# Kernel tuning notes

Measured on AMD Instinct MI355X. Metric: run time of the kernel, lower is better.

## Reference

```python
import jax, jax.numpy as jnp
import numpy as np

NUM_ENT = 40000
NUM_REL = 100
EMBED_DIM = 256
FEAT_DIM = 768
BATCH = 32
SEQ_LEN = 3
MASK_POS = 2
EPS = 1e-12


def setup_inputs() -> dict:
    key = jax.random.key(0)
    k1, k2, k3, k4 = jax.random.split(key, 4)
    ent_pkl = jax.random.normal(k1, (NUM_ENT, FEAT_DIM), dtype=jnp.float32)
    other_emb = jax.random.normal(k2, (NUM_ENT + NUM_REL + 3 - NUM_ENT, EMBED_DIM), dtype=jnp.float32)
    proj_W = jax.random.normal(k3, (EMBED_DIM, FEAT_DIM), dtype=jnp.float32) * (1.0 / np.sqrt(FEAT_DIM))
    batch_input_ids = jax.random.randint(k4, (BATCH, SEQ_LEN), 0, NUM_ENT + NUM_REL + 3, dtype=jnp.int64)
    return {
        "ent_pkl": ent_pkl,
        "other_emb": other_emb,
        "proj_W": proj_W,
        "batch_input_ids": batch_input_ids,
        "batch_mask_position": MASK_POS,
    }


def reference(ent_pkl, other_emb, proj_W, batch_input_ids, batch_mask_position):
    # unity embeddings: [other[0], proj(ent_pkl), other[1:]] -> [num_ent+num_rel+3, d]
    ent_proj = ent_pkl @ proj_W.T  # Linear(feat_dim, embed_dim, bias=False)
    unity = jnp.concatenate([other_emb[:1], ent_proj, other_emb[1:]], axis=0)

    mp = int(batch_mask_position)
    # drop the masked slot, keep up to 3 tokens total -> [B, 2]
    query_input = jnp.concatenate(
        [batch_input_ids[:, :mp], batch_input_ids[:, mp + 1:3]], axis=1)
    query_emb = unity[query_input]  # [B, 2, d]
    # F.normalize(dim=-1): x / max(||x||_2, eps)
    norm = jnp.sqrt(jnp.sum(query_emb * query_emb, axis=-1, keepdims=True))
    query_emb = query_emb / jnp.maximum(norm, EPS)
    query_sum = jnp.sum(query_emb, axis=1)  # [B, d]

    E_embed = unity[:NUM_ENT + 1]  # [num_ent+1, d]
    # broadcast L1 distance: [B, num_ent+1]
    score = -jnp.sum(jnp.abs(query_sum[:, None, :] - E_embed[None, :, :]), axis=-1)
    return score
```

## Files before the change

### kernel.cpp

```cpp
#include <hip/hip_runtime.h>
#include <hip/hip_bf16.h>
#include <stdint.h>

#define NE 40000
#define FD 768
#define ED 256
#define NB 32
#define OUTC (NE + 1)

typedef __bf16 bf16x8 __attribute__((ext_vector_type(8)));
typedef float f32x4 __attribute__((ext_vector_type(4)));
typedef float f32x16 __attribute__((ext_vector_type(16)));

#define WS_QS 0
#define WS_N01 (32 * 1024)
#define WS_WB (96 * 1024)

__device__ __forceinline__ float bflo(unsigned u) {
    union { unsigned u; float f; } v; v.u = u << 16; return v.f;
}
__device__ __forceinline__ float bfhi(unsigned u) {
    union { unsigned u; float f; } v; v.u = u & 0xffff0000u; return v.f;
}

__global__ __launch_bounds__(256) void prep_kernel(
    const float* __restrict__ ent_pkl, const float* __restrict__ W,
    const int* __restrict__ ids, const int* __restrict__ mpos,
    __bf16* __restrict__ Wb, float* __restrict__ n01_raw)
{
    const int bid = blockIdx.x;
    const int t = threadIdx.x;

    if (bid < 192) {
        int i = bid * 1024 + t * 4;
        float4 v = *(const float4*)(W + i);
        __bf16 o[4] = {(__bf16)v.x, (__bf16)v.y, (__bf16)v.z, (__bf16)v.w};
        *(ushort4*)(Wb + i) = *(const ushort4*)o;
        return;
    }

    __shared__ float row[FD];
    const int slot = bid - 192;
    const int b = slot >> 1, s = slot & 1;
    const int mp = mpos[0];
    const int col = (s < mp) ? s : s + 1;
    const bool wide = (ids[1] == 0 && ids[3] == 0 && ids[5] == 0);
    const int flat = b * 3 + col;
    const int idx = wide ? ids[flat * 2] : ids[flat];
    if (!(idx >= 1 && idx <= NE)) return;

    const float* src = ent_pkl + (size_t)(idx - 1) * FD;
    for (int k = t; k < FD; k += 256) row[k] = src[k];
    __syncthreads();

    const float4* w4 = (const float4*)(W + (size_t)t * FD);
    const float4* r4 = (const float4*)row;
    float a0 = 0.f, a1 = 0.f, a2 = 0.f, a3 = 0.f;
#pragma unroll 2
    for (int k4 = 0; k4 < FD / 4; k4 += 4) {
        float4 w0 = w4[k4 + 0], r0 = r4[k4 + 0];
        float4 w1 = w4[k4 + 1], r1 = r4[k4 + 1];
        float4 w2 = w4[k4 + 2], r2 = r4[k4 + 2];
        float4 w3 = w4[k4 + 3], r3 = r4[k4 + 3];
        a0 += w0.x * r0.x + w0.y * r0.y + w0.z * r0.z + w0.w * r0.w;
        a1 += w1.x * r1.x + w1.y * r1.y + w1.z * r1.z + w1.w * r1.w;
        a2 += w2.x * r2.x + w2.y * r2.y + w2.z * r2.z + w2.w * r2.w;
        a3 += w3.x * r3.x + w3.y * r3.y + w3.z * r3.z + w3.w * r3.w;
    }
    n01_raw[slot * ED + t] = (a0 + a1) + (a2 + a3);
}

__global__ __launch_bounds__(256) void qsum_kernel(
    const float* __restrict__ other_emb, const float* __restrict__ n01_raw,
    const int* __restrict__ ids, const int* __restrict__ mpos,
    float* __restrict__ qs, float* __restrict__ out)
{
    __shared__ float red[4];
    __shared__ float nshare;
    const int b = blockIdx.x, t = threadIdx.x;
    const int mp = mpos[0];
    const bool wide = (ids[1] == 0 && ids[3] == 0 && ids[5] == 0);

    float q = 0.f;
#pragma unroll
    for (int s = 0; s < 2; ++s) {
        const int col = (s < mp) ? s : s + 1;
        const int flat = b * 3 + col;
        const int idx = wide ? ids[flat * 2] : ids[flat];
        float v;
        if (idx >= 1 && idx <= NE) v = n01_raw[(b * 2 + s) * ED + t];
        else if (idx == 0) v = other_emb[t];
        else v = other_emb[(size_t)(idx - NE) * ED + t];

        float ss = v * v;
#pragma unroll
        for (int o = 32; o > 0; o >>= 1) ss += __shfl_down(ss, o, 64);
        if ((t & 63) == 0) red[t >> 6] = ss;
        __syncthreads();
        if (t == 0) nshare = fmaxf(sqrtf(red[0] + red[1] + red[2] + red[3]), 1e-12f);
        __syncthreads();
        q += v / nshare;
        __syncthreads();
    }
    qs[b * ED + t] = q;

    float d = fabsf(q - other_emb[t]);
#pragma unroll
    for (int o = 32; o > 0; o >>= 1) d += __shfl_down(d, o, 64);
    if ((t & 63) == 0) red[t >> 6] = d;
    __syncthreads();
    if (t == 0) out[(size_t)b * OUTC] = -(red[0] + red[1] + red[2] + red[3]);
}

#define SP 264

__global__ __launch_bounds__(512, 6) void gemm_score_kernel(
    const float* __restrict__ ent_pkl, const __bf16* __restrict__ Wb,
    const float* __restrict__ qs, float* __restrict__ out)
{
    __shared__ __align__(16) unsigned char smem[49152];
    __bf16* Asm = (__bf16*)smem;
    __bf16* Sb = (__bf16*)smem;

    const int t = threadIdx.x;
    const int l = t & 63;
    const int w = t >> 6;
    const int m31 = l & 31;
    const int dh = l >> 5;
    const int e0 = blockIdx.x * 64;

    f32x16 acc0 = {0.f}, acc1 = {0.f};
#pragma unroll
    for (int i = 0; i < 16; ++i) { acc0[i] = 0.f; acc1[i] = 0.f; }

    const int srow = t >> 3;
    const int sseg = t & 7;
    const int ssw = srow & 7;
    const __bf16* brow = Wb + (size_t)(32 * w + m31) * FD + dh * 8;
    const __bf16* arow0 = Asm + m31 * 384;
    const __bf16* arow1 = Asm + (32 + m31) * 384;
    const int asw = m31 & 7;

#pragma unroll
    for (int h = 0; h < 2; ++h) {
        __syncthreads();
        {
            const float* ap = ent_pkl + (size_t)(e0 + srow) * FD + h * 384 + sseg * 48;
            __bf16* dst = Asm + srow * 384;
#pragma unroll
            for (int j = 0; j < 6; ++j) {
                float4 x = *(const float4*)(ap + j * 8);
                float4 y = *(const float4*)(ap + j * 8 + 4);
                bf16x8 v;
                v[0] = (__bf16)x.x; v[1] = (__bf16)x.y; v[2] = (__bf16)x.z; v[3] = (__bf16)x.w;
                v[4] = (__bf16)y.x; v[5] = (__bf16)y.y; v[6] = (__bf16)y.z; v[7] = (__bf16)y.w;
                *(bf16x8*)(dst + ((sseg * 6 + j) ^ ssw) * 8) = v;
            }
        }
        __syncthreads();
#pragma unroll 4
        for (int c = 0; c < 24; ++c) {
            bf16x8 bv = *(const bf16x8*)(brow + h * 384 + c * 16);
            const int oct = (2 * c + dh) ^ asw;
            bf16x8 a0 = *(const bf16x8*)(arow0 + oct * 8);
            bf16x8 a1 = *(const bf16x8*)(arow1 + oct * 8);
            acc0 = __builtin_amdgcn_mfma_f32_32x32x16_bf16(a0, bv, acc0, 0, 0, 0);
            acc1 = __builtin_amdgcn_mfma_f32_32x32x16_bf16(a1, bv, acc1, 0, 0, 0);
        }
    }

    __syncthreads();
#pragma unroll
    for (int r = 0; r < 16; ++r) {
        const int erow = (r & 3) + 8 * (r >> 2) + 4 * dh;
        Sb[erow * SP + 32 * w + m31] = (__bf16)acc0[r];
        Sb[(32 + erow) * SP + 32 * w + m31] = (__bf16)acc1[r];
    }
    __syncthreads();

    const int wu = __builtin_amdgcn_readfirstlane(w);
    const float4* q0 = (const float4*)(qs + (4 * wu + 0) * ED);
    const float4* q1 = (const float4*)(qs + (4 * wu + 1) * ED);
    const float4* q2 = (const float4*)(qs + (4 * wu + 2) * ED);
    const float4* q3 = (const float4*)(qs + (4 * wu + 3) * ED);
    const unsigned* xrow = (const unsigned*)(Sb + l * SP);

    float s0 = 0.f, s1 = 0.f, s2 = 0.f, s3 = 0.f;
#pragma unroll 2
    for (int c = 0; c < 64; ++c) {
        uint2 xd = *(const uint2*)(xrow + c * 2);
        float x0 = bflo(xd.x), x1 = bfhi(xd.x);
        float x2 = bflo(xd.y), x3 = bfhi(xd.y);
        float4 qa = q0[c];
        float4 qb = q1[c];
        float4 qc = q2[c];
        float4 qd = q3[c];
        s0 += fabsf(qa.x - x0) + fabsf(qa.y - x1) + fabsf(qa.z - x2) + fabsf(qa.w - x3);
        s1 += fabsf(qb.x - x0) + fabsf(qb.y - x1) + fabsf(qb.z - x2) + fabsf(qb.w - x3);
        s2 += fabsf(qc.x - x0) + fabsf(qc.y - x1) + fabsf(qc.z - x2) + fabsf(qc.w - x3);
        s3 += fabsf(qd.x - x0) + fabsf(qd.y - x1) + fabsf(qd.z - x2) + fabsf(qd.w - x3);
    }
    float* ob = out + 1 + e0 + l;
    ob[(size_t)(4 * wu + 0) * OUTC] = -s0;
    ob[(size_t)(4 * wu + 1) * OUTC] = -s1;
    ob[(size_t)(4 * wu + 2) * OUTC] = -s2;
    ob[(size_t)(4 * wu + 3) * OUTC] = -s3;
}

extern "C" void kernel_launch(void* const* d_in, const int* in_sizes, int n_in,
                              void* d_out, int out_size, void* d_ws, size_t ws_size,
                              hipStream_t stream) {
    const float* ent_pkl = (const float*)d_in[0];
    const float* other_emb = (const float*)d_in[1];
    const float* proj_W = (const float*)d_in[2];
    const int* ids = (const int*)d_in[3];
    const int* mpos = (const int*)d_in[4];
    float* out = (float*)d_out;

    float* qs = (float*)((char*)d_ws + WS_QS);
    float* n01_raw = (float*)((char*)d_ws + WS_N01);
    __bf16* Wb = (__bf16*)((char*)d_ws + WS_WB);

    prep_kernel<<<256, 256, 0, stream>>>(ent_pkl, proj_W, ids, mpos, Wb, n01_raw);
    qsum_kernel<<<NB, 256, 0, stream>>>(other_emb, n01_raw, ids, mpos, qs, out);
    gemm_score_kernel<<<NE / 64, 512, 0, stream>>>(ent_pkl, Wb, qs, out);
}
```

Baseline: 262.1 us.

## Use packed fp16 L1 scoring, fragment-ordered weight layout, and nontemporal streaming

The L1-distance epilogue now runs in packed half precision. Projected entity rows are stored as fp16 in shared memory, the query sums are kept as fp16, and the absolute differences are accumulated in f16x2 over blocks of 8 chunks before being widened to fp32. The bf16 weight copy is rearranged into the MFMA fragment order so each lane does one contiguous 16-byte load. Entity features are read and scores written with nontemporal hints. The aim is to halve the ALU work in the scoring loop and make weight loads coalesced, at the cost of fp16 accumulation error in the partial sums.

Result: slower. 278.4 us (+6.2%).

```diff
diff --git a/kernel.cpp b/kernel.cpp
--- a/kernel.cpp
+++ b/kernel.cpp
@@ -11,36 +11,43 @@
 typedef __bf16 bf16x8 __attribute__((ext_vector_type(8)));
 typedef float f32x4 __attribute__((ext_vector_type(4)));
 typedef float f32x16 __attribute__((ext_vector_type(16)));
+typedef _Float16 f16x2 __attribute__((ext_vector_type(2)));
+typedef _Float16 f16x4 __attribute__((ext_vector_type(4)));
 
 #define WS_QS 0
 #define WS_N01 (32 * 1024)
 #define WS_WB (96 * 1024)
 
-__device__ __forceinline__ float bflo(unsigned u) {
-    union { unsigned u; float f; } v; v.u = u << 16; return v.f;
-}
-__device__ __forceinline__ float bfhi(unsigned u) {
-    union { unsigned u; float f; } v; v.u = u & 0xffff0000u; return v.f;
+__device__ __forceinline__ f16x2 pabs2(f16x2 d) {
+    union { f16x2 h; unsigned u; } v; v.h = d; v.u &= 0x7FFF7FFFu; return v.h;
 }
 
 __global__ __launch_bounds__(256) void prep_kernel(
     const float* __restrict__ ent_pkl, const float* __restrict__ W,
     const int* __restrict__ ids, const int* __restrict__ mpos,
-    __bf16* __restrict__ Wb, float* __restrict__ n01_raw)
+    __bf16* __restrict__ Wf, float* __restrict__ n01_raw)
 {
     const int bid = blockIdx.x;
     const int t = threadIdx.x;
 
-    if (bid < 192) {
-        int i = bid * 1024 + t * 4;
-        float4 v = *(const float4*)(W + i);
-        __bf16 o[4] = {(__bf16)v.x, (__bf16)v.y, (__bf16)v.z, (__bf16)v.w};
-        *(ushort4*)(Wb + i) = *(const ushort4*)o;
+    if (bid < 96) {
+        const int f = bid * 256 + t;
+        const int w = f / 3072;
+        const int r = f - w * 3072;
+        const int g = r >> 6;
+        const int l = r & 63;
+        const float* src = W + (size_t)(32 * w + (l & 31)) * FD + g * 16 + (l >> 5) * 8;
+        float4 a = *(const float4*)src;
+        float4 b = *(const float4*)(src + 4);
+        bf16x8 v;
+        v[0] = (__bf16)a.x; v[1] = (__bf16)a.y; v[2] = (__bf16)a.z; v[3] = (__bf16)a.w;
+        v[4] = (__bf16)b.x; v[5] = (__bf16)b.y; v[6] = (__bf16)b.z; v[7] = (__bf16)b.w;
+        *(bf16x8*)(Wf + (size_t)f * 8) = v;
         return;
     }
 
     __shared__ float row[FD];
-    const int slot = bid - 192;
+    const int slot = bid - 96;
     const int b = slot >> 1, s = slot & 1;
     const int mp = mpos[0];
     const int col = (s < mp) ? s : s + 1;
@@ -73,7 +80,7 @@
 __global__ __launch_bounds__(256) void qsum_kernel(
     const float* __restrict__ other_emb, const float* __restrict__ n01_raw,
     const int* __restrict__ ids, const int* __restrict__ mpos,
-    float* __restrict__ qs, float* __restrict__ out)
+    _Float16* __restrict__ qh, float* __restrict__ out)
 {
     __shared__ float red[4];
     __shared__ float nshare;
@@ -102,7 +109,7 @@
         q += v / nshare;
         __syncthreads();
     }
-    qs[b * ED + t] = q;
+    qh[b * ED + t] = (_Float16)q;
 
     float d = fabsf(q - other_emb[t]);
 #pragma unroll
@@ -112,15 +119,15 @@
     if (t == 0) out[(size_t)b * OUTC] = -(red[0] + red[1] + red[2] + red[3]);
 }
 
-#define SP 264
+#define SP 260
 
 __global__ __launch_bounds__(512, 6) void gemm_score_kernel(
-    const float* __restrict__ ent_pkl, const __bf16* __restrict__ Wb,
-    const float* __restrict__ qs, float* __restrict__ out)
+    const float* __restrict__ ent_pkl, const __bf16* __restrict__ Wf,
+    const _Float16* __restrict__ qh, float* __restrict__ out)
 {
     __shared__ __align__(16) unsigned char smem[49152];
     __bf16* Asm = (__bf16*)smem;
-    __bf16* Sb = (__bf16*)smem;
+    _Float16* Sb = (_Float16*)smem;
 
     const int t = threadIdx.x;
     const int l = t & 63;
@@ -129,14 +136,14 @@
     const int dh = l >> 5;
     const int e0 = blockIdx.x * 64;
 
-    f32x16 acc0 = {0.f}, acc1 = {0.f};
+    f32x16 acc0, acc1;
 #pragma unroll
     for (int i = 0; i < 16; ++i) { acc0[i] = 0.f; acc1[i] = 0.f; }
 
     const int srow = t >> 3;
     const int sseg = t & 7;
     const int ssw = srow & 7;
-    const __bf16* brow = Wb + (size_t)(32 * w + m31) * FD + dh * 8;
+    const __bf16* bp = Wf + (size_t)w * 24576 + (size_t)l * 8;
     const __bf16* arow0 = Asm + m31 * 384;
     const __bf16* arow1 = Asm + (32 + m31) * 384;
     const int asw = m31 & 7;
@@ -146,21 +153,22 @@
         __syncthreads();
         {
             const float* ap = ent_pkl + (size_t)(e0 + srow) * FD + h * 384 + sseg * 48;
+            const f32x4* ap4 = (const f32x4*)ap;
             __bf16* dst = Asm + srow * 384;
 #pragma unroll
             for (int j = 0; j < 6; ++j) {
-                float4 x = *(const float4*)(ap + j * 8);
-                float4 y = *(const float4*)(ap + j * 8 + 4);
+                f32x4 x = __builtin_nontemporal_load(ap4 + 2 * j);
+                f32x4 y = __builtin_nontemporal_load(ap4 + 2 * j + 1);
                 bf16x8 v;
-                v[0] = (__bf16)x.x; v[1] = (__bf16)x.y; v[2] = (__bf16)x.z; v[3] = (__bf16)x.w;
-                v[4] = (__bf16)y.x; v[5] = (__bf16)y.y; v[6] = (__bf16)y.z; v[7] = (__bf16)y.w;
+                v[0] = (__bf16)x[0]; v[1] = (__bf16)x[1]; v[2] = (__bf16)x[2]; v[3] = (__bf16)x[3];
+                v[4] = (__bf16)y[0]; v[5] = (__bf16)y[1]; v[6] = (__bf16)y[2]; v[7] = (__bf16)y[3];
                 *(bf16x8*)(dst + ((sseg * 6 + j) ^ ssw) * 8) = v;
             }
         }
         __syncthreads();
 #pragma unroll 4
         for (int c = 0; c < 24; ++c) {
-            bf16x8 bv = *(const bf16x8*)(brow + h * 384 + c * 16);
+            bf16x8 bv = *(const bf16x8*)(bp + (size_t)(h * 24 + c) * 512);
             const int oct = (2 * c + dh) ^ asw;
             bf16x8 a0 = *(const bf16x8*)(arow0 + oct * 8);
             bf16x8 a1 = *(const bf16x8*)(arow1 + oct * 8);
@@ -173,38 +181,47 @@
 #pragma unroll
     for (int r = 0; r < 16; ++r) {
         const int erow = (r & 3) + 8 * (r >> 2) + 4 * dh;
-        Sb[erow * SP + 32 * w + m31] = (__bf16)acc0[r];
-        Sb[(32 + erow) * SP + 32 * w + m31] = (__bf16)acc1[r];
+        Sb[erow * SP + 32 * w + m31] = (_Float16)acc0[r];
+        Sb[(32 + erow) * SP + 32 * w + m31] = (_Float16)acc1[r];
     }
     __syncthreads();
 
     const int wu = __builtin_amdgcn_readfirstlane(w);
-    const float4* q0 = (const float4*)(qs + (4 * wu + 0) * ED);
-    const float4* q1 = (const float4*)(qs + (4 * wu + 1) * ED);
-    const float4* q2 = (const float4*)(qs + (4 * wu + 2) * ED);
-    const float4* q3 = (const float4*)(qs + (4 * wu + 3) * ED);
-    const unsigned* xrow = (const unsigned*)(Sb + l * SP);
+    const f16x4* q0 = (const f16x4*)(qh + (size_t)(4 * wu + 0) * ED);
+    const f16x4* q1 = (const f16x4*)(qh + (size_t)(4 * wu + 1) * ED);
+    const f16x4* q2 = (const f16x4*)(qh + (size_t)(4 * wu + 2) * ED);
+    const f16x4* q3 = (const f16x4*)(qh + (size_t)(4 * wu + 3) * ED);
+    const f16x4* xrow = (const f16x4*)(Sb + (size_t)l * SP);
 
     float s0 = 0.f, s1 = 0.f, s2 = 0.f, s3 = 0.f;
-#pragma unroll 2
-    for (int c = 0; c < 64; ++c) {
-        uint2 xd = *(const uint2*)(xrow + c * 2);
-        float x0 = bflo(xd.x), x1 = bfhi(xd.x);
-        float x2 = bflo(xd.y), x3 = bfhi(xd.y);
-        float4 qa = q0[c];
-        float4 qb = q1[c];
-        float4 qc = q2[c];
-        float4 qd = q3[c];
-        s0 += fabsf(qa.x - x0) + fabsf(qa.y - x1) + fabsf(qa.z - x2) + fabsf(qa.w - x3);
-        s1 += fabsf(qb.x - x0) + fabsf(qb.y - x1) + fabsf(qb.z - x2) + fabsf(qb.w - x3);
-        s2 += fabsf(qc.x - x0) + fabsf(qc.y - x1) + fabsf(qc.z - x2) + fabsf(qc.w - x3);
-        s3 += fabsf(qd.x - x0) + fabsf(qd.y - x1) + fabsf(qd.z - x2) + fabsf(qd.w - x3);
+    for (int cb = 0; cb < 8; ++cb) {
+        f16x2 t0 = {0, 0}, t1 = {0, 0}, t2 = {0, 0}, t3 = {0, 0};
+#pragma unroll
+        for (int ci = 0; ci < 8; ++ci) {
+            const int c = cb * 8 + ci;
+            f16x4 xv = xrow[c];
+            f16x2 xlo = __builtin_shufflevector(xv, xv, 0, 1);
+            f16x2 xhi = __builtin_shufflevector(xv, xv, 2, 3);
+            f16x4 qa = q0[c], qb = q1[c], qc = q2[c], qd = q3[c];
+            t0 = t0 + pabs2(__builtin_shufflevector(qa, qa, 0, 1) - xlo);
+            t0 = t0 + pabs2(__builtin_shufflevector(qa, qa, 2, 3) - xhi);
+            t1 = t1 + pabs2(__builtin_shufflevector(qb, qb, 0, 1) - xlo);
+            t1 = t1 + pabs2(__builtin_shufflevector(qb, qb, 2, 3) - xhi);
+            t2 = t2 + pabs2(__builtin_shufflevector(qc, qc, 0, 1) - xlo);
+            t2 = t2 + pabs2(__builtin_shufflevector(qc, qc, 2, 3) - xhi);
+            t3 = t3 + pabs2(__builtin_shufflevector(qd, qd, 0, 1) - xlo);
+            t3 = t3 + pabs2(__builtin_shufflevector(qd, qd, 2, 3) - xhi);
+        }
+        s0 += (float)t0[0] + (float)t0[1];
+        s1 += (float)t1[0] + (float)t1[1];
+        s2 += (float)t2[0] + (float)t2[1];
+        s3 += (float)t3[0] + (float)t3[1];
     }
     float* ob = out + 1 + e0 + l;
-    ob[(size_t)(4 * wu + 0) * OUTC] = -s0;
-    ob[(size_t)(4 * wu + 1) * OUTC] = -s1;
-    ob[(size_t)(4 * wu + 2) * OUTC] = -s2;
-    ob[(size_t)(4 * wu + 3) * OUTC] = -s3;
+    __builtin_nontemporal_store(-s0, ob + (size_t)(4 * wu + 0) * OUTC);
+    __builtin_nontemporal_store(-s1, ob + (size_t)(4 * wu + 1) * OUTC);
+    __builtin_nontemporal_store(-s2, ob + (size_t)(4 * wu + 2) * OUTC);
+    __builtin_nontemporal_store(-s3, ob + (size_t)(4 * wu + 3) * OUTC);
 }
 
 extern "C" void kernel_launch(void* const* d_in, const int* in_sizes, int n_in,
@@ -217,11 +234,11 @@
     const int* mpos = (const int*)d_in[4];
     float* out = (float*)d_out;
 
-    float* qs = (float*)((char*)d_ws + WS_QS);
+    _Float16* qh = (_Float16*)((char*)d_ws + WS_QS);
     float* n01_raw = (float*)((char*)d_ws + WS_N01);
-    __bf16* Wb = (__bf16*)((char*)d_ws + WS_WB);
-
-    prep_kernel<<<256, 256, 0, stream>>>(ent_pkl, proj_W, ids, mpos, Wb, n01_raw);
-    qsum_kernel<<<NB, 256, 0, stream>>>(other_emb, n01_raw, ids, mpos, qs, out);
-    gemm_score_kernel<<<NE / 64, 512, 0, stream>>>(ent_pkl, Wb, qs, out);
-}
+    __bf16* Wf = (__bf16*)((char*)d_ws + WS_WB);
+
+    prep_kernel<<<160, 256, 0, stream>>>(ent_pkl, proj_W, ids, mpos, Wf, n01_raw);
+    qsum_kernel<<<NB, 256, 0, stream>>>(other_emb, n01_raw, ids, mpos, qh, out);
+    gemm_score_kernel<<<NE / 64, 512, 0, stream>>>(ent_pkl, Wf, qh, out);
+}
```
